# Kernel optimization log

Hardware: AMD Instinct MI355X
Metric: run time of the kernel (lower is better)

Reference implementation:

```python
import jax, jax.numpy as jnp
import numpy as np

S_, T_, F_, SF_, G_ = 16, 400, 16, 250, 4  # systems, time, features, shuffleFactor, feature groups


def setup_inputs() -> dict:
    key = jax.random.key(0)
    ks = jax.random.split(key, 10)
    observations = jax.random.normal(ks[0], (S_, T_, F_), dtype=jnp.float32)
    mu = 0.1 * jax.random.normal(ks[1], (F_, 1), dtype=jnp.float32)
    Sigma_minus_half = (0.1 * jax.random.normal(ks[2], (F_, F_), dtype=jnp.float32)
                        + jnp.eye(F_, dtype=jnp.float32))
    # true random permutations of the time axis, per (shuffle-rep, feature-group, system)
    perm_idx = jnp.argsort(jax.random.uniform(ks[3], (SF_, G_, S_, T_)), axis=-1).astype(jnp.int32)
    W1 = jax.random.normal(ks[4], (F_, 32), dtype=jnp.float32) / jnp.sqrt(F_)
    b1 = jnp.zeros((32,), jnp.float32)
    W2 = jax.random.normal(ks[5], (32, 16), dtype=jnp.float32) / jnp.sqrt(32.0)
    b2 = jnp.zeros((16,), jnp.float32)
    W3 = jax.random.normal(ks[6], (16, 1), dtype=jnp.float32) / 4.0
    b3 = jnp.zeros((1,), jnp.float32)
    return dict(observations=observations, mu=mu, Sigma_minus_half=Sigma_minus_half,
                perm_idx=perm_idx, W1=W1, b1=b1, W2=W2, b2=b2, W3=W3, b3=b3)


def reference(observations, mu, Sigma_minus_half, perm_idx, W1, b1, W2, b2, W3, b3):
    # --- multipleShuffles: per-system, per-feature-group time permutation, repeated SF_ times ---
    feat_group = jnp.repeat(jnp.arange(G_), F_ // G_)          # [F] feature -> group id
    p = perm_idx[:, feat_group]                                 # [SF, F, S, T]
    p = jnp.transpose(p, (2, 0, 3, 1)).astype(jnp.int32)        # [S, SF, T, F]
    shuf = jnp.take_along_axis(observations[:, None, :, :], p, axis=2)  # [S, SF, T, F]
    shuf = shuf.reshape(S_, SF_ * T_, F_)                       # [S, SF*T, F]

    # --- normalizeObservations: Sigma^{-1/2} @ (z - mu) applied per (system, time) ---
    def normalize(x):
        return jnp.einsum('ij,stj->sti', Sigma_minus_half, x - mu[:, 0])

    # --- sequence MLP: Linear(F,32)-LeakyReLU-Linear(32,16)-LeakyReLU-Linear(16,1)-Sigmoid ---
    def mlp(x):
        h = jax.nn.leaky_relu(x @ W1 + b1, negative_slope=0.01)
        h = jax.nn.leaky_relu(h @ W2 + b2, negative_slope=0.01)
        return jax.nn.sigmoid(h @ W3 + b3)

    comb = mlp(normalize(observations))      # [S, T, 1]
    comb_shuf = mlp(normalize(shuf))         # [S, SF*T, 1]
    return jnp.concatenate([comb, comb_shuf], axis=1)  # [S, T*(1+SF), 1]
```

## Files before the change

kernel.cpp:

```cpp
#include <hip/hip_runtime.h>
#include <hip/hip_fp16.h>

#define S_N 16
#define T_N 400
#define F_N 16
#define SF_N 250
#define G_N 4
#define OUT_ROW 100400

typedef _Float16 f16x8 __attribute__((ext_vector_type(8)));
typedef float    f32x4 __attribute__((ext_vector_type(4)));

union QU { uint4 u; f16x8 v; };

#define QTAB_OFF   0
#define W2FRAG_OFF 1638400
#define B1H_OFF    1639424
#define B2F_OFF    1639488
#define W3F_OFF    1639552
#define B3F_OFF    1639616

__global__ __launch_bounds__(64) void precompute_kernel(
    const float* __restrict__ obs,
    const float* __restrict__ mu,
    const float* __restrict__ Sig,
    const float* __restrict__ W1,
    const float* __restrict__ b1,
    const float* __restrict__ W2,
    const float* __restrict__ b2,
    const float* __restrict__ W3,
    const float* __restrict__ b3,
    __half* __restrict__ qtab,
    __half* __restrict__ w2frag,
    __half* __restrict__ b1h,
    float* __restrict__ b2f,
    float* __restrict__ w3f,
    float* __restrict__ b3f,
    float* __restrict__ out)
{
    __shared__ float sAm[512];
    __shared__ float sW2[512];
    __shared__ float sMu[16];
    __shared__ float sB1[32];
    __shared__ float sB2[16];
    __shared__ float sW3[16];
    __shared__ float sB3;

    const int tid = threadIdx.x;

    for (int e = tid; e < 512; e += 64) {
        int j = e >> 5, k = e & 31;
        float acc = 0.f;
        #pragma unroll
        for (int i = 0; i < 16; ++i)
            acc = fmaf(Sig[i * 16 + j], W1[i * 32 + k], acc);
        sAm[e] = acc;
        sW2[e] = W2[e];
    }
    if (tid < 16) sMu[tid] = mu[tid];
    if (tid < 32) sB1[tid] = b1[tid];
    if (tid < 16) sB2[tid] = b2[tid];
    if (tid < 16) sW3[tid] = W3[tid];
    if (tid == 0) sB3 = b3[0];
    __syncthreads();

    if (blockIdx.x == 0) {
        {
            int n = tid & 15, cc = tid >> 4;
            #pragma unroll
            for (int j = 0; j < 8; ++j)
                w2frag[tid * 8 + j] = __float2half(sW2[(cc * 8 + j) * 16 + n]);
        }
        if (tid < 32) b1h[tid] = __float2half(sB1[tid]);
        if (tid < 16) b2f[tid] = sB2[tid];
        if (tid < 16) w3f[tid] = sW3[tid];
        if (tid == 0) b3f[0] = sB3;
    }

    const int gid = blockIdx.x * 64 + tid;
    const int s = gid / T_N;
    const int t = gid - s * T_N;

    float xm[16];
    {
        const float4* op = (const float4*)(obs + (size_t)gid * 16);
        float4 o0 = op[0], o1 = op[1], o2 = op[2], o3 = op[3];
        float v[16] = {o0.x, o0.y, o0.z, o0.w, o1.x, o1.y, o1.z, o1.w,
                       o2.x, o2.y, o2.z, o2.w, o3.x, o3.y, o3.z, o3.w};
        #pragma unroll
        for (int j = 0; j < 16; ++j) xm[j] = v[j] - sMu[j];
    }

    float h1[32];
    #pragma unroll
    for (int k = 0; k < 32; ++k) h1[k] = sB1[k];

    #pragma unroll
    for (int g = 0; g < 4; ++g) {
        float qg[32];
        #pragma unroll
        for (int k = 0; k < 32; ++k) {
            float a = xm[4 * g + 0] * sAm[(4 * g + 0) * 32 + k];
            a = fmaf(xm[4 * g + 1], sAm[(4 * g + 1) * 32 + k], a);
            a = fmaf(xm[4 * g + 2], sAm[(4 * g + 2) * 32 + k], a);
            a = fmaf(xm[4 * g + 3], sAm[(4 * g + 3) * 32 + k], a);
            qg[k] = a;
            h1[k] += a;
        }
        __half2* dst = (__half2*)(qtab + ((size_t)(s * 4 + g) * T_N + t) * 32);
        #pragma unroll
        for (int k2 = 0; k2 < 16; ++k2)
            dst[k2] = __floats2half2_rn(qg[2 * k2], qg[2 * k2 + 1]);
    }

    #pragma unroll
    for (int k = 0; k < 32; ++k) h1[k] = fmaxf(h1[k], 0.01f * h1[k]);

    float h2[16];
    #pragma unroll
    for (int j = 0; j < 16; ++j) h2[j] = sB2[j];
    #pragma unroll
    for (int k = 0; k < 32; ++k) {
        float a = h1[k];
        #pragma unroll
        for (int j = 0; j < 16; ++j) h2[j] = fmaf(a, sW2[k * 16 + j], h2[j]);
    }
    float acc = sB3;
    #pragma unroll
    for (int j = 0; j < 16; ++j) {
        float hj = fmaxf(h2[j], 0.01f * h2[j]);
        acc = fmaf(hj, sW3[j], acc);
    }
    out[(size_t)s * OUT_ROW + t] = 1.f / (1.f + __expf(-acc));
}

__global__ __launch_bounds__(256, 4) void eval_kernel(
    const int* __restrict__ perm,
    const __half* __restrict__ qtab,
    const __half* __restrict__ w2frag,
    const __half* __restrict__ b1h,
    const float* __restrict__ b2f,
    const float* __restrict__ w3f,
    const float* __restrict__ b3p,
    float* __restrict__ out)
{
    const int tid  = threadIdx.x;
    const int lane = tid & 63;
    const int m    = lane & 15;
    const int c    = lane >> 4;
    const int base = (blockIdx.x * 4 + (tid >> 6)) * 64;

    int pidx[4];
    int s_q[4];
    #pragma unroll
    for (int q = 0; q < 4; ++q) {
        const int e_m = base + q * 16 + m;
        const int s   = e_m / 100000;
        const int r1  = e_m - s * 100000;
        const int sf  = r1 / 400;
        const int t   = r1 - sf * 400;
        s_q[q] = s;
        pidx[q] = perm[sf * 25600 + c * 6400 + s * 400 + t];
    }

    const f16x8 afrag = *(const f16x8*)(w2frag + lane * 8);
    const f16x8 b1v   = *(const f16x8*)(b1h + c * 8);
    const float4 b2v  = *(const float4*)(b2f + c * 4);
    const float4 w3v  = *(const float4*)(w3f + c * 4);
    const float  b3   = b3p[0];

    int idx[4][4];
    #pragma unroll
    for (int q = 0; q < 4; ++q) {
        idx[q][0] = __shfl(pidx[q], m);
        idx[q][1] = __shfl(pidx[q], 16 + m);
        idx[q][2] = __shfl(pidx[q], 32 + m);
        idx[q][3] = __shfl(pidx[q], 48 + m);
    }

    QU a[4][4];
    #pragma unroll
    for (int q = 0; q < 4; ++q) {
        const size_t rb = (size_t)s_q[q] * 1600;
        #pragma unroll
        for (int g = 0; g < 4; ++g)
            a[q][g].u = *(const uint4*)(qtab + (rb + g * 400 + idx[q][g]) * 32 + c * 8);
    }

    float res0, res1, res2, res3;
    #pragma unroll
    for (int q = 0; q < 4; ++q) {
        f16x8 h = (a[q][0].v + a[q][1].v) + (a[q][2].v + a[q][3].v) + b1v;
        #pragma unroll
        for (int k = 0; k < 8; ++k) {
            _Float16 x = h[k];
            _Float16 y = x * (_Float16)0.01f;
            h[k] = x > y ? x : y;
        }

        f32x4 acc = {0.f, 0.f, 0.f, 0.f};
        acc = __builtin_amdgcn_mfma_f32_16x16x32_f16(afrag, h, acc, 0, 0, 0);

        float p;
        {
            float v0 = acc[0] + b2v.x; v0 = fmaxf(v0, 0.01f * v0); p = v0 * w3v.x;
            float v1 = acc[1] + b2v.y; v1 = fmaxf(v1, 0.01f * v1); p = fmaf(v1, w3v.y, p);
            float v2 = acc[2] + b2v.z; v2 = fmaxf(v2, 0.01f * v2); p = fmaf(v2, w3v.z, p);
            float v3 = acc[3] + b2v.w; v3 = fmaxf(v3, 0.01f * v3); p = fmaf(v3, w3v.w, p);
        }
        p += __shfl_xor(p, 16);
        p += __shfl_xor(p, 32);
        if (q == 0) res0 = p;
        else if (q == 1) res1 = p;
        else if (q == 2) res2 = p;
        else res3 = p;
    }

    float v = res0;
    if (c == 1) v = res1;
    if (c == 2) v = res2;
    if (c == 3) v = res3;
    v += b3;
    const float sg = 1.f / (1.f + __expf(-v));
    const int e_s = base + lane;
    const int s2  = e_s / 100000;
    const int r2  = e_s - s2 * 100000;
    out[(size_t)s2 * OUT_ROW + 400 + r2] = sg;
}

extern "C" void kernel_launch(void* const* d_in, const int* in_sizes, int n_in,
                              void* d_out, int out_size, void* d_ws, size_t ws_size,
                              hipStream_t stream) {
    (void)in_sizes; (void)n_in; (void)out_size; (void)ws_size;
    const float* obs = (const float*)d_in[0];
    const float* mu  = (const float*)d_in[1];
    const float* Sig = (const float*)d_in[2];
    const int*   prm = (const int*)d_in[3];
    const float* W1  = (const float*)d_in[4];
    const float* b1  = (const float*)d_in[5];
    const float* W2  = (const float*)d_in[6];
    const float* b2  = (const float*)d_in[7];
    const float* W3  = (const float*)d_in[8];
    const float* b3  = (const float*)d_in[9];

    char* ws = (char*)d_ws;
    __half* qtab   = (__half*)(ws + QTAB_OFF);
    __half* w2frag = (__half*)(ws + W2FRAG_OFF);
    __half* b1h    = (__half*)(ws + B1H_OFF);
    float*  b2f    = (float*)(ws + B2F_OFF);
    float*  w3f    = (float*)(ws + W3F_OFF);
    float*  b3f    = (float*)(ws + B3F_OFF);
    float*  out    = (float*)d_out;

    hipLaunchKernelGGL(precompute_kernel, dim3(100), dim3(64), 0, stream,
                       obs, mu, Sig, W1, b1, W2, b2, W3, b3,
                       qtab, w2frag, b1h, b2f, w3f, b3f, out);
    hipLaunchKernelGGL(eval_kernel, dim3(6250), dim3(256), 0, stream,
                       prm, qtab, w2frag, b1h, b2f, w3f, b3f, out);
}
```

Measured before the change: 129.8 us.

## Stage per-system q-table in LDS and gather permuted rows from shared memory

The eval kernel now launches one 1024-thread block per (system, chunk). Each block first copies that system's 1600x32 half q-table (100 KB) into LDS, padded to a stride of 5 uint4 to avoid bank conflicts. Wavefronts then loop over 64-element tiles and gather the permuted rows from LDS instead of doing random global loads. Permutation indices are read directly from global memory rather than through lane shuffles. This removes scattered global/L2 traffic, but it adds a 100 KB LDS staging cost per block, 16x redundant staging per system, low occupancy (one block per CU), and fewer blocks overall.

```diff
diff --git a/kernel.cpp b/kernel.cpp
--- a/kernel.cpp
+++ b/kernel.cpp
@@ -19,6 +19,8 @@
 #define B2F_OFF    1639488
 #define W3F_OFF    1639552
 #define B3F_OFF    1639616
+
+#define LDS_U4     8000
 
 __global__ __launch_bounds__(64) void precompute_kernel(
     const float* __restrict__ obs,
@@ -134,7 +136,7 @@
     out[(size_t)s * OUT_ROW + t] = 1.f / (1.f + __expf(-acc));
 }
 
-__global__ __launch_bounds__(256, 4) void eval_kernel(
+__global__ __launch_bounds__(1024, 4) void eval_kernel(
     const int* __restrict__ perm,
     const __half* __restrict__ qtab,
     const __half* __restrict__ w2frag,
@@ -144,24 +146,24 @@
     const float* __restrict__ b3p,
     float* __restrict__ out)
 {
-    const int tid  = threadIdx.x;
+    extern __shared__ uint4 smem[];
+
+    const int tid   = threadIdx.x;
+    const int s     = blockIdx.x >> 4;
+    const int chunk = blockIdx.x & 15;
+    const int j0b   = chunk * 6250;
+
+    const uint4* qsrc = (const uint4*)(qtab + (size_t)s * 1600 * 32);
+    for (int e = tid; e < 6400; e += 1024) {
+        int r = e >> 2, cc = e & 3;
+        smem[r * 5 + cc] = qsrc[e];
+    }
+    __syncthreads();
+
     const int lane = tid & 63;
+    const int wv   = tid >> 6;
     const int m    = lane & 15;
     const int c    = lane >> 4;
-    const int base = (blockIdx.x * 4 + (tid >> 6)) * 64;
-
-    int pidx[4];
-    int s_q[4];
-    #pragma unroll
-    for (int q = 0; q < 4; ++q) {
-        const int e_m = base + q * 16 + m;
-        const int s   = e_m / 100000;
-        const int r1  = e_m - s * 100000;
-        const int sf  = r1 / 400;
-        const int t   = r1 - sf * 400;
-        s_q[q] = s;
-        pidx[q] = perm[sf * 25600 + c * 6400 + s * 400 + t];
-    }
 
     const f16x8 afrag = *(const f16x8*)(w2frag + lane * 8);
     const f16x8 b1v   = *(const f16x8*)(b1h + c * 8);
@@ -169,63 +171,68 @@
     const float4 w3v  = *(const float4*)(w3f + c * 4);
     const float  b3   = b3p[0];
 
-    int idx[4][4];
-    #pragma unroll
-    for (int q = 0; q < 4; ++q) {
-        idx[q][0] = __shfl(pidx[q], m);
-        idx[q][1] = __shfl(pidx[q], 16 + m);
-        idx[q][2] = __shfl(pidx[q], 32 + m);
-        idx[q][3] = __shfl(pidx[q], 48 + m);
-    }
-
-    QU a[4][4];
-    #pragma unroll
-    for (int q = 0; q < 4; ++q) {
-        const size_t rb = (size_t)s_q[q] * 1600;
-        #pragma unroll
-        for (int g = 0; g < 4; ++g)
-            a[q][g].u = *(const uint4*)(qtab + (rb + g * 400 + idx[q][g]) * 32 + c * 8);
-    }
-
-    float res0, res1, res2, res3;
-    #pragma unroll
-    for (int q = 0; q < 4; ++q) {
-        f16x8 h = (a[q][0].v + a[q][1].v) + (a[q][2].v + a[q][3].v) + b1v;
-        #pragma unroll
-        for (int k = 0; k < 8; ++k) {
-            _Float16 x = h[k];
-            _Float16 y = x * (_Float16)0.01f;
-            h[k] = x > y ? x : y;
-        }
-
-        f32x4 acc = {0.f, 0.f, 0.f, 0.f};
-        acc = __builtin_amdgcn_mfma_f32_16x16x32_f16(afrag, h, acc, 0, 0, 0);
-
-        float p;
-        {
-            float v0 = acc[0] + b2v.x; v0 = fmaxf(v0, 0.01f * v0); p = v0 * w3v.x;
-            float v1 = acc[1] + b2v.y; v1 = fmaxf(v1, 0.01f * v1); p = fmaf(v1, w3v.y, p);
-            float v2 = acc[2] + b2v.z; v2 = fmaxf(v2, 0.01f * v2); p = fmaf(v2, w3v.z, p);
-            float v3 = acc[3] + b2v.w; v3 = fmaxf(v3, 0.01f * v3); p = fmaf(v3, w3v.w, p);
-        }
-        p += __shfl_xor(p, 16);
-        p += __shfl_xor(p, 32);
-        if (q == 0) res0 = p;
-        else if (q == 1) res1 = p;
-        else if (q == 2) res2 = p;
-        else res3 = p;
-    }
-
-    float v = res0;
-    if (c == 1) v = res1;
-    if (c == 2) v = res2;
-    if (c == 3) v = res3;
-    v += b3;
-    const float sg = 1.f / (1.f + __expf(-v));
-    const int e_s = base + lane;
-    const int s2  = e_s / 100000;
-    const int r2  = e_s - s2 * 100000;
-    out[(size_t)s2 * OUT_ROW + 400 + r2] = sg;
+    for (int tile = wv; tile < 98; tile += 16) {
+        const int jt = j0b + tile * 64;
+
+        int idx[4][4];
+        #pragma unroll
+        for (int q = 0; q < 4; ++q) {
+            int j = jt + q * 16 + m;
+            int jc = j0b + 6249;
+            if (j < jc) jc = j;
+            const int sf = jc / 400;
+            const int t  = jc - sf * 400;
+            const int pb = sf * 25600 + s * 400 + t;
+            #pragma unroll
+            for (int g = 0; g < 4; ++g)
+                idx[q][g] = perm[pb + g * 6400];
+        }
+
+        float res0, res1, res2, res3;
+        #pragma unroll
+        for (int q = 0; q < 4; ++q) {
+            QU a0, a1, a2, a3;
+            a0.u = smem[(idx[q][0]         ) * 5 + c];
+            a1.u = smem[( 400 + idx[q][1]  ) * 5 + c];
+            a2.u = smem[( 800 + idx[q][2]  ) * 5 + c];
+            a3.u = smem[(1200 + idx[q][3]  ) * 5 + c];
+
+            f16x8 h = (a0.v + a1.v) + (a2.v + a3.v) + b1v;
+            #pragma unroll
+            for (int k = 0; k < 8; ++k) {
+                _Float16 x = h[k];
+                _Float16 y = x * (_Float16)0.01f;
+                h[k] = x > y ? x : y;
+            }
+
+            f32x4 acc = {0.f, 0.f, 0.f, 0.f};
+            acc = __builtin_amdgcn_mfma_f32_16x16x32_f16(afrag, h, acc, 0, 0, 0);
+
+            float p;
+            {
+                float v0 = acc[0] + b2v.x; v0 = fmaxf(v0, 0.01f * v0); p = v0 * w3v.x;
+                float v1 = acc[1] + b2v.y; v1 = fmaxf(v1, 0.01f * v1); p = fmaf(v1, w3v.y, p);
+                float v2 = acc[2] + b2v.z; v2 = fmaxf(v2, 0.01f * v2); p = fmaf(v2, w3v.z, p);
+                float v3 = acc[3] + b2v.w; v3 = fmaxf(v3, 0.01f * v3); p = fmaf(v3, w3v.w, p);
+            }
+            p += __shfl_xor(p, 16);
+            p += __shfl_xor(p, 32);
+            if (q == 0) res0 = p;
+            else if (q == 1) res1 = p;
+            else if (q == 2) res2 = p;
+            else res3 = p;
+        }
+
+        float v = res0;
+        if (c == 1) v = res1;
+        if (c == 2) v = res2;
+        if (c == 3) v = res3;
+        v += b3;
+        const float sg = 1.f / (1.f + __expf(-v));
+        const int j = jt + lane;
+        if (j < j0b + 6250)
+            out[(size_t)s * OUT_ROW + 400 + j] = sg;
+    }
 }
 
 extern "C" void kernel_launch(void* const* d_in, const int* in_sizes, int n_in,
@@ -252,9 +259,13 @@
     float*  b3f    = (float*)(ws + B3F_OFF);
     float*  out    = (float*)d_out;
 
+    (void)hipFuncSetAttribute((const void*)eval_kernel,
+                              hipFuncAttributeMaxDynamicSharedMemorySize,
+                              LDS_U4 * 16);
+
     hipLaunchKernelGGL(precompute_kernel, dim3(100), dim3(64), 0, stream,
                        obs, mu, Sig, W1, b1, W2, b2, W3, b3,
                        qtab, w2frag, b1h, b2f, w3f, b3f, out);
-    hipLaunchKernelGGL(eval_kernel, dim3(6250), dim3(256), 0, stream,
+    hipLaunchKernelGGL(eval_kernel, dim3(256), dim3(1024), LDS_U4 * 16, stream,
                        prm, qtab, w2frag, b1h, b2f, w3f, b3f, out);
 }
```

New measurement: 117.2 us. -9.7%, faster.
